# Kernel tuning notes

Hardware: AMD Instinct MI355X
Metric: run time of the kernel (lower is better)

Reference implementation:

```python
import jax, jax.numpy as jnp
import numpy as np

N, D_IN, D_OUT = 4096, 1024, 1024

def setup_inputs() -> dict:
    key = jax.random.key(0)
    k1, k2, k3, k4 = jax.random.split(key, 4)
    x = jax.random.normal(k1, (N, D_IN), dtype=jnp.float32)
    # original uses torch.rand (uniform [0,1)) for params
    w_query = jax.random.uniform(k2, (D_IN, D_OUT), dtype=jnp.float32)
    w_key = jax.random.uniform(k3, (D_IN, D_OUT), dtype=jnp.float32)
    w_value = jax.random.uniform(k4, (D_IN, D_OUT), dtype=jnp.float32)
    return {"x": x, "w_query": w_query, "w_key": w_key, "w_value": w_value}

def reference(x, w_query, w_key, w_value):
    queries = x @ w_query          # [N, d_out]
    keys = x @ w_key               # [N, d_out]
    values = x @ w_value           # [N, d_out]
    scale = keys.shape[-1] ** 0.5
    scores = queries @ keys.T      # [N, N]
    attn = jax.nn.softmax(scores / scale, axis=-1)
    return attn @ values           # [N, d_out]
```

## Files before the change

kernel.cpp:

```cpp
#include <hip/hip_runtime.h>
#include <math.h>

#define NROWS 4096
#define DDIM  1024

typedef __attribute__((ext_vector_type(8))) short short8;
typedef __attribute__((ext_vector_type(4))) float f32x4;

__device__ __forceinline__ ushort f2bf(float v) {
  union { float f; uint32_t u; } c; c.f = v;
  uint32_t u = c.u;
  uint32_t lsb = (u >> 16) & 1u;
  u += 0x7fffu + lsb;
  return (ushort)(u >> 16);
}
__device__ __forceinline__ float bf2f(ushort h) {
  union { uint32_t u; float f; } c; c.u = ((uint32_t)h) << 16;
  return c.f;
}

__device__ __forceinline__ void gll16(const void* g, void* l) {
  __builtin_amdgcn_global_load_lds((const __attribute__((address_space(1))) void*)g,
                                   (__attribute__((address_space(3))) void*)l, 16, 0, 0);
}

__device__ __forceinline__ size_t pidx(int r, int c, int ldt) {
  return ((size_t)((r >> 4) * ldt + (c >> 5))) * 512 +
         ((c >> 3) & 3) * 128 + (r & 15) * 8 + (c & 7);
}
__device__ __forceinline__ size_t pidxs(int r, int c, int ldt) {
  return ((size_t)((r >> 4) * ldt + (c >> 5))) * 1024 +
         ((c >> 3) & 3) * 128 + (r & 15) * 8 + (c & 7);
}

__global__ __launch_bounds__(256) void prep(const float* __restrict__ x,
                                            const float* __restrict__ wq,
                                            const float* __restrict__ wk,
                                            const float* __restrict__ wv,
                                            ushort* Xc,
                                            ushort* Wqc, ushort* Wkc, ushort* Wvh) {
  __shared__ float tl[32][33];
  const int b = blockIdx.x, t = threadIdx.x;
  if (b < 1024) {
    const f32x4* src = (const f32x4*)x;
#pragma unroll
    for (int r = 0; r < 4; ++r) {
      int i = b * 1024 + r * 256 + t;
      int row = i >> 8;
      int c = (i & 255) << 2;
      f32x4 v = __builtin_nontemporal_load(src + i);
      ushort4 h, l;
      h.x = f2bf(v.x); l.x = f2bf(v.x - bf2f(h.x));
      h.y = f2bf(v.y); l.y = f2bf(v.y - bf2f(h.y));
      h.z = f2bf(v.z); l.z = f2bf(v.z - bf2f(h.z));
      h.w = f2bf(v.w); l.w = f2bf(v.w - bf2f(h.w));
      size_t o = pidxs(row, c, DDIM / 32);
      *(ushort4*)(Xc + o) = h;
      *(ushort4*)(Xc + o + 512) = l;
    }
  } else {
    const int z = (b - 1024) >> 10;
    const int tile = (b - 1024) & 1023;
    const float* src = z == 0 ? wq : (z == 1 ? wk : wv);
    const int r0 = (tile >> 5) * 32;
    const int c0 = (tile & 31) * 32;
    const int tx = t & 31, ty = t >> 5;
    for (int i = ty; i < 32; i += 8)
      tl[i][tx] = __builtin_nontemporal_load(&src[(size_t)(r0 + i) * DDIM + c0 + tx]);
    __syncthreads();
    if (z == 2) {
      for (int i = ty; i < 32; i += 8) {
        float v = tl[tx][i];
        Wvh[pidx(c0 + i, r0 + tx, DDIM / 32)] = f2bf(v);
      }
    } else {
      ushort* d = z == 0 ? Wqc : Wkc;
      for (int i = ty; i < 32; i += 8) {
        float v = tl[tx][i];
        ushort h = f2bf(v);
        size_t o = pidxs(c0 + i, r0 + tx, DDIM / 32);
        d[o] = h;
        d[o + 512] = f2bf(v - bf2f(h));
      }
    }
  }
}

template <int MI, bool SPLIT, int KT, int KTOT, int SA, int SB>
__device__ __forceinline__ void direct_gemm(const ushort* __restrict__ A,
                                            const ushort* __restrict__ B,
                                            int m0, int n0, f32x4 (*acc)[4]) {
  const int t = threadIdx.x;
  const int wv = t >> 6, ln = t & 63;
  const int arb = (wv >> 1) * (MI * 16), crb = (wv & 1) * 64;
  const int ra = (m0 + arb) >> 4;
  const int rb = (n0 + crb) >> 4;

  uint oA[MI], oB[4];
#pragma unroll
  for (int i = 0; i < MI; ++i) oA[i] = (uint)(ra + i) * (uint)(KTOT * SA) + (uint)ln * 8u;
#pragma unroll
  for (int j = 0; j < 4; ++j) oB[j] = (uint)(rb + j) * (uint)(KTOT * SB) + (uint)ln * 8u;

  short8 ah0[MI], al0[MI], bh0[4], bl0[4];
  short8 ah1[MI], al1[MI], bh1[4], bl1[4];

#define DG_LOAD(sidx, AH, AL, BH, BL)                                        \
  {                                                                          \
    uint sa_ = (uint)(sidx) * (uint)SA;                                      \
    uint sb_ = (uint)(sidx) * (uint)SB;                                      \
    _Pragma("unroll") for (int i_ = 0; i_ < MI; ++i_) {                      \
      const ushort* pa_ = A + oA[i_] + sa_;                                  \
      AH[i_] = *(const short8*)pa_;                                          \
      if constexpr (SPLIT) AL[i_] = *(const short8*)(pa_ + 512);             \
    }                                                                        \
    _Pragma("unroll") for (int j_ = 0; j_ < 4; ++j_) {                       \
      const ushort* pb_ = B + oB[j_] + sb_;                                  \
      BH[j_] = *(const short8*)pb_;                                          \
      if constexpr (SPLIT) BL[j_] = *(const short8*)(pb_ + 512);             \
    }                                                                        \
  }

#define DG_MFMA(AH, AL, BH, BL)                                              \
  {                                                                          \
    __builtin_amdgcn_s_setprio(1);                                           \
    _Pragma("unroll") for (int j_ = 0; j_ < 4; ++j_) {                       \
      _Pragma("unroll") for (int i_ = 0; i_ < MI; ++i_) {                    \
        acc[i_][j_] = __builtin_amdgcn_mfma_f32_16x16x32_bf16(               \
            AH[i_], BH[j_], acc[i_][j_], 0, 0, 0);                           \
        if constexpr (SPLIT) {                                               \
          acc[i_][j_] = __builtin_amdgcn_mfma_f32_16x16x32_bf16(             \
              AH[i_], BL[j_], acc[i_][j_], 0, 0, 0);                         \
          acc[i_][j_] = __builtin_amdgcn_mfma_f32_16x16x32_bf16(             \
              AL[i_], BH[j_], acc[i_][j_], 0, 0, 0);                         \
        }                                                                    \
      }                                                                      \
    }                                                                        \
    __builtin_amdgcn_s_setprio(0);                                           \
  }

  DG_LOAD(0, ah0, al0, bh0, bl0);
#pragma unroll 1
  for (int s = 0; s < KT - 2; s += 2) {
    DG_LOAD(s + 1, ah1, al1, bh1, bl1);
    DG_MFMA(ah0, al0, bh0, bl0);
    DG_LOAD(s + 2, ah0, al0, bh0, bl0);
    DG_MFMA(ah1, al1, bh1, bl1);
  }
  DG_LOAD(KT - 1, ah1, al1, bh1, bl1);
  DG_MFMA(ah0, al0, bh0, bl0);
  DG_MFMA(ah1, al1, bh1, bl1);

#undef DG_LOAD
#undef DG_MFMA
}

__global__ __launch_bounds__(256) void gemm_qkv(const ushort* __restrict__ Xc,
                                                const ushort* __restrict__ Wqc,
                                                const ushort* __restrict__ Wkc,
                                                const ushort* __restrict__ Wvh,
                                                ushort* Qc, ushort* Kc, ushort* Vt) {
  __shared__ char smem[2][32768];
  const int bid = blockIdx.x;
  const int which = bid >> 8;
  const int local = bid & 255;
  const int xcd = local & 7, idx = local >> 3;
  const int t = threadIdx.x;
  const int w = t >> 6, ln = t & 63;
  const int wr = w >> 1, wc = w & 1;
  const int quad = ln >> 4, l16 = ln & 15;

  f32x4 acc[4][4];
#pragma unroll
  for (int i = 0; i < 4; ++i)
#pragma unroll
    for (int j = 0; j < 4; ++j) acc[i][j] = (f32x4){0.f, 0.f, 0.f, 0.f};

  if (which < 2) {
    const int m0 = (xcd * 4 + (idx >> 3)) * 128;
    const int n0 = (idx & 7) * 128;
    const ushort* Bc = which ? Wkc : Wqc;
    const char* srcBase = (w < 2)
        ? (const char*)Xc + (size_t)((m0 >> 4) + (w & 1) * 4) * 65536
        : (const char*)Bc + (size_t)((n0 >> 4) + (w & 1) * 4) * 65536;
    srcBase += ln * 16;
    char* ldsBase = (char*)smem + (w < 2 ? 0 : 16384) + (w & 1) * 8192 + ln * 16;

#pragma unroll
    for (int u = 0; u < 8; ++u)
      gll16(srcBase + (u >> 1) * 65536 + (u & 1) * 1024, ldsBase + u * 1024);
    asm volatile("s_waitcnt vmcnt(0)" ::: "memory");
    __builtin_amdgcn_s_barrier();

    const char* aB = (char*)smem + wr * 8192 + ln * 16;
    const char* bB = (char*)smem + 16384 + wc * 8192 + ln * 16;

#pragma unroll 1
    for (int kt = 0; kt < 32; ++kt) {
      const int cb = (kt & 1) << 15;
      const int nb = ((kt + 1) & 1) << 15;
      if (kt < 31) {
        const char* srcK = srcBase + (size_t)(kt + 1) * 2048;
#pragma unroll
        for (int u = 0; u < 8; ++u)
          gll16(srcK + (u >> 1) * 65536 + (u & 1) * 1024, ldsBase + nb + u * 1024);
      }

      short8 bh[4], bl[4];
#pragma unroll
      for (int j = 0; j < 4; ++j) {
        bh[j] = *(const short8*)(bB + cb + j * 2048);
        bl[j] = *(const short8*)(bB + cb + j * 2048 + 1024);
      }
      __builtin_amdgcn_s_setprio(1);
#pragma unroll
      for (int i = 0; i < 4; ++i) {
        short8 ah = *(const short8*)(aB + cb + i * 2048);
        short8 al = *(const short8*)(aB + cb + i * 2048 + 1024);
#pragma unroll
        for (int j = 0; j < 4; ++j) {
          acc[i][j] = __builtin_amdgcn_mfma_f32_16x16x32_bf16(ah, bh[j], acc[i][j], 0, 0, 0);
          acc[i][j] = __builtin_amdgcn_mfma_f32_16x16x32_bf16(ah, bl[j], acc[i][j], 0, 0, 0);
          acc[i][j] = __builtin_amdgcn_mfma_f32_16x16x32_bf16(al, bh[j], acc[i][j], 0, 0, 0);
        }
      }
      __builtin_amdgcn_s_setprio(0);

      asm volatile("s_waitcnt vmcnt(0)" ::: "memory");
      __builtin_amdgcn_s_barrier();
    }

    const float scale = which ? 1.0f : 0.03125f;
    ushort* D = which ? Kc : Qc;
#pragma unroll
    for (int i = 0; i < 4; ++i)
#pragma unroll
      for (int j = 0; j < 4; ++j) {
        int col = n0 + wc * 64 + j * 16 + l16;
        int rw = m0 + wr * 64 + i * 16 + quad * 4;
#pragma unroll
        for (int r2 = 0; r2 < 4; ++r2) {
          float v = acc[i][j][r2] * scale;
          ushort h = f2bf(v);
          size_t o = pidxs(rw + r2, col, DDIM / 32);
          D[o] = h;
          D[o + 512] = f2bf(v - bf2f(h));
        }
      }
  } else {
    const int m0 = (idx & 7) * 128;
    const int n0 = (xcd * 4 + (idx >> 3)) * 128;
    const char* srcBase = (w < 2)
        ? (const char*)Wvh + (size_t)((m0 >> 4) + (w & 1) * 4) * 32768
        : (const char*)Xc + (size_t)((n0 >> 4) + (w & 1) * 4) * 65536;
    srcBase += ln * 16;
    char* ldsBase = (char*)smem + (w < 2 ? 0 : 8192) + (w & 1) * 4096 + ln * 16;
    const size_t srcStep = (w < 2) ? 1024 : 2048;
    const size_t rowStr = (w < 2) ? 32768 : 65536;

#pragma unroll
    for (int u = 0; u < 4; ++u)
      gll16(srcBase + (size_t)u * rowStr, ldsBase + u * 1024);
    asm volatile("s_waitcnt vmcnt(0)" ::: "memory");
    __builtin_amdgcn_s_barrier();

    const char* aB = (char*)smem + wr * 4096 + ln * 16;
    const char* bB = (char*)smem + 8192 + wc * 4096 + ln * 16;

#pragma unroll 1
    for (int kt = 0; kt < 32; ++kt) {
      const int cb = (kt & 1) << 15;
      const int nb = ((kt + 1) & 1) << 15;
      if (kt < 31) {
        const char* srcK = srcBase + (size_t)(kt + 1) * srcStep;
#pragma unroll
        for (int u = 0; u < 4; ++u)
          gll16(srcK + (size_t)u * rowStr, ldsBase + nb + u * 1024);
      }

      short8 bh[4];
#pragma unroll
      for (int j = 0; j < 4; ++j)
        bh[j] = *(const short8*)(bB + cb + j * 1024);
      __builtin_amdgcn_s_setprio(1);
#pragma unroll
      for (int i = 0; i < 4; ++i) {
        short8 ah = *(const short8*)(aB + cb + i * 1024);
#pragma unroll
        for (int j = 0; j < 4; ++j)
          acc[i][j] = __builtin_amdgcn_mfma_f32_16x16x32_bf16(ah, bh[j], acc[i][j], 0, 0, 0);
      }
      __builtin_amdgcn_s_setprio(0);

      asm volatile("s_waitcnt vmcnt(0)" ::: "memory");
      __builtin_amdgcn_s_barrier();
    }

#pragma unroll
    for (int i = 0; i < 4; ++i)
#pragma unroll
      for (int j = 0; j < 4; ++j) {
        int kv = n0 + wc * 64 + j * 16 + l16;
        int d = m0 + wr * 64 + i * 16 + quad * 4;
#pragma unroll
        for (int r2 = 0; r2 < 4; ++r2)
          Vt[pidx(d + r2, kv, NROWS / 32)] = f2bf(acc[i][j][r2]);
      }
  }
}

__global__ __launch_bounds__(512) void gemm_s(const ushort* __restrict__ Qc,
                                              const ushort* __restrict__ Kc,
                                              float* __restrict__ S) {
  __shared__ char smem[2][65536];
  const int bid = blockIdx.y * 16 + blockIdx.x;
  const int xcd = bid & 7, local = bid >> 3;
  const int m0 = ((xcd >> 1) * 4 + (local & 3)) * 256;
  const int n0 = ((xcd & 1) * 8 + (local >> 2)) * 256;
  const int t = threadIdx.x;
  const int w = t >> 6, ln = t & 63;
  const int wr = w >> 2, wc = w & 3;
  const int quad = ln >> 4, l16 = ln & 15;

  const char* srcBase = (w < 4)
      ? (const char*)Qc + (size_t)((m0 >> 4) + w * 4) * 65536
      : (const char*)Kc + (size_t)((n0 >> 4) + (w - 4) * 4) * 65536;
  srcBase += ln * 16;
  char* ldsBase = (char*)smem + w * 8192 + ln * 16;

  f32x4 acc[8][4];
#pragma unroll
  for (int i = 0; i < 8; ++i)
#pragma unroll
    for (int j = 0; j < 4; ++j) acc[i][j] = (f32x4){0.f, 0.f, 0.f, 0.f};

#pragma unroll
  for (int u = 0; u < 8; ++u)
    gll16(srcBase + (u >> 1) * 65536 + (u & 1) * 1024, ldsBase + u * 1024);
  asm volatile("s_waitcnt vmcnt(0)" ::: "memory");
  __builtin_amdgcn_s_barrier();

  const char* aB = (char*)smem + (wr * 8) * 2048 + ln * 16;
  const char* bB = (char*)smem + 32768 + (wc * 4) * 2048 + ln * 16;

#pragma unroll 1
  for (int kt = 0; kt < 32; ++kt) {
    const int cb = (kt & 1) << 16;
    const int nb = ((kt + 1) & 1) << 16;
    const char* srcK = srcBase + (size_t)(kt + 1) * 2048;

    if (kt < 31) {
#pragma unroll
      for (int u = 0; u < 8; ++u)
        gll16(srcK + (u >> 1) * 65536 + (u & 1) * 1024, ldsBase + nb + u * 1024);
    }

    short8 bh[4], bl[4];
#pragma unroll
    for (int j = 0; j < 4; ++j) {
      bh[j] = *(const short8*)(bB + cb + j * 2048);
      bl[j] = *(const short8*)(bB + cb + j * 2048 + 1024);
    }

#pragma unroll
    for (int p = 0; p < 4; ++p) {
      short8 ah0 = *(const short8*)(aB + cb + (2 * p) * 2048);
      short8 al0 = *(const short8*)(aB + cb + (2 * p) * 2048 + 1024);
      short8 ah1 = *(const short8*)(aB + cb + (2 * p + 1) * 2048);
      short8 al1 = *(const short8*)(aB + cb + (2 * p + 1) * 2048 + 1024);
      __builtin_amdgcn_s_setprio(1);
#pragma unroll
      for (int j_ = 0; j_ < 4; ++j_) {
        acc[2 * p][j_] = __builtin_amdgcn_mfma_f32_16x16x32_bf16(ah0, bh[j_], acc[2 * p][j_], 0, 0, 0);
        acc[2 * p][j_] = __builtin_amdgcn_mfma_f32_16x16x32_bf16(ah0, bl[j_], acc[2 * p][j_], 0, 0, 0);
        acc[2 * p][j_] = __builtin_amdgcn_mfma_f32_16x16x32_bf16(al0, bh[j_], acc[2 * p][j_], 0, 0, 0);
        acc[2 * p + 1][j_] = __builtin_amdgcn_mfma_f32_16x16x32_bf16(ah1, bh[j_], acc[2 * p + 1][j_], 0, 0, 0);
        acc[2 * p + 1][j_] = __builtin_amdgcn_mfma_f32_16x16x32_bf16(ah1, bl[j_], acc[2 * p + 1][j_], 0, 0, 0);
        acc[2 * p + 1][j_] = __builtin_amdgcn_mfma_f32_16x16x32_bf16(al1, bh[j_], acc[2 * p + 1][j_], 0, 0, 0);
      }
      __builtin_amdgcn_s_setprio(0);
    }

    asm volatile("s_waitcnt vmcnt(0)" ::: "memory");
    __builtin_amdgcn_s_barrier();
  }

#pragma unroll
  for (int i = 0; i < 8; ++i)
#pragma unroll
    for (int j = 0; j < 4; ++j) {
      int col = n0 + wc * 64 + j * 16 + l16;
      int rw = m0 + wr * 128 + i * 16 + quad * 4;
#pragma unroll
      for (int r2 = 0; r2 < 4; ++r2)
        S[(size_t)(rw + r2) * NROWS + col] = acc[i][j][r2];
    }
}

__global__ __launch_bounds__(256) void softmax_pack(const float* __restrict__ S,
                                                    ushort* __restrict__ P) {
  const int row = blockIdx.x, t = threadIdx.x;
  const float* Sr = S + (size_t)row * NROWS;
  const f32x4* S4 = (const f32x4*)Sr;
  f32x4 v[4];
  float mx = -3.4e38f;
#pragma unroll
  for (int c = 0; c < 4; ++c) {
    v[c] = S4[c * 256 + t];
    mx = fmaxf(mx, fmaxf(fmaxf(v[c].x, v[c].y), fmaxf(v[c].z, v[c].w)));
  }
  __shared__ float red[4];
  for (int o = 32; o >= 1; o >>= 1) mx = fmaxf(mx, __shfl_xor(mx, o));
  int wv = t >> 6, ln = t & 63;
  if (ln == 0) red[wv] = mx;
  __syncthreads();
  mx = fmaxf(fmaxf(red[0], red[1]), fmaxf(red[2], red[3]));
  float s = 0.f;
#pragma unroll
  for (int c = 0; c < 4; ++c) {
    v[c].x = __expf(v[c].x - mx);
    v[c].y = __expf(v[c].y - mx);
    v[c].z = __expf(v[c].z - mx);
    v[c].w = __expf(v[c].w - mx);
    s += v[c].x + v[c].y + v[c].z + v[c].w;
  }
  for (int o = 32; o >= 1; o >>= 1) s += __shfl_xor(s, o);
  __syncthreads();
  if (ln == 0) red[wv] = s;
  __syncthreads();
  s = red[0] + red[1] + red[2] + red[3];
  float inv = 1.f / s;
#pragma unroll
  for (int c = 0; c < 4; ++c) {
    ushort4 h;
    h.x = f2bf(v[c].x * inv);
    h.y = f2bf(v[c].y * inv);
    h.z = f2bf(v[c].z * inv);
    h.w = f2bf(v[c].w * inv);
    int c0 = 1024 * c + 4 * t;
    *(ushort4*)(P + pidx(row, c0, NROWS / 32)) = h;
  }
}

__global__ __launch_bounds__(256) void gemm_pv(const ushort* __restrict__ P,
                                               const ushort* __restrict__ Vt,
                                               float* __restrict__ Out) {
  const int n0 = blockIdx.x * 128, m0 = blockIdx.y * 128;
  const int t = threadIdx.x;
  const int wv = t >> 6, ln = t & 63;
  const int quad = ln >> 4, l16 = ln & 15;

  f32x4 acc[4][4];
#pragma unroll
  for (int i = 0; i < 4; ++i)
#pragma unroll
    for (int j = 0; j < 4; ++j) acc[i][j] = (f32x4){0.f, 0.f, 0.f, 0.f};

  direct_gemm<4, false, 128, 128, 512, 512>(P, Vt, m0, n0, acc);

#pragma unroll
  for (int i = 0; i < 4; ++i)
#pragma unroll
    for (int j = 0; j < 4; ++j) {
      int col = n0 + (wv & 1) * 64 + j * 16 + l16;
      int rw = m0 + (wv >> 1) * 64 + i * 16 + quad * 4;
#pragma unroll
      for (int r2 = 0; r2 < 4; ++r2)
        Out[(size_t)(rw + r2) * DDIM + col] = acc[i][j][r2];
    }
}

extern "C" void kernel_launch(void* const* d_in, const int* in_sizes, int n_in,
                              void* d_out, int out_size, void* d_ws, size_t ws_size,
                              hipStream_t stream) {
  const float* x  = (const float*)d_in[0];
  const float* wq = (const float*)d_in[1];
  const float* wk = (const float*)d_in[2];
  const float* wv = (const float*)d_in[3];
  char* ws = (char*)d_ws;
  const size_t MB = 1u << 20;

  ushort* Vt  = (ushort*)(ws + 0);
  ushort* Qc  = (ushort*)(ws + 8 * MB);
  ushort* Kc  = (ushort*)(ws + 24 * MB);
  ushort* Pp  = (ushort*)(ws + 8 * MB);
  ushort* Xc  = (ushort*)(ws + 40 * MB);
  ushort* Wqc = (ushort*)(ws + 56 * MB);
  ushort* Wkc = (ushort*)(ws + 60 * MB);
  ushort* Wvh = (ushort*)(ws + 64 * MB);
  float*  S   = (float*)(ws + 40 * MB);
  float*  Out = (float*)d_out;

  prep<<<4096, 256, 0, stream>>>(x, wq, wk, wv, Xc, Wqc, Wkc, Wvh);
  gemm_qkv<<<768, 256, 0, stream>>>(Xc, Wqc, Wkc, Wvh, Qc, Kc, Vt);
  gemm_s<<<dim3(16, 16), 512, 0, stream>>>(Qc, Kc, S);
  softmax_pack<<<NROWS, 256, 0, stream>>>(S, Pp);
  gemm_pv<<<dim3(8, 32), 256, 0, stream>>>(Pp, Vt, Out);
}
```

Before: 300.5 us.

## Coalesce packed-layout writes via LDS staging and change P layout for PV GEMM

The prep kernel now stages the hi/lo bf16 splits of x and the weights in shared memory, so each block writes whole packed tiles with wide contiguous stores instead of scattered 2-byte and 8-byte writes. Softmax now writes P in a k-tile-major layout with contiguous 16-byte row chunks, and gemm_pv gets its own inlined loader matched to that layout. The gemm_qkv block order is also permuted so the V blocks are scheduled first. These changes target uncoalesced global stores in the pack stages, at the cost of extra LDS traffic and barriers.

```diff
diff --git a/kernel.cpp b/kernel.cpp
--- a/kernel.cpp
+++ b/kernel.cpp
@@ -39,28 +39,45 @@
                                             const float* __restrict__ wv,
                                             ushort* Xc,
                                             ushort* Wqc, ushort* Wkc, ushort* Wvh) {
-  __shared__ float tl[32][33];
+  __shared__ char smem[8448];
   const int b = blockIdx.x, t = threadIdx.x;
-  if (b < 1024) {
-    const f32x4* src = (const f32x4*)x;
-#pragma unroll
-    for (int r = 0; r < 4; ++r) {
-      int i = b * 1024 + r * 256 + t;
-      int row = i >> 8;
-      int c = (i & 255) << 2;
-      f32x4 v = __builtin_nontemporal_load(src + i);
-      ushort4 h, l;
-      h.x = f2bf(v.x); l.x = f2bf(v.x - bf2f(h.x));
-      h.y = f2bf(v.y); l.y = f2bf(v.y - bf2f(h.y));
-      h.z = f2bf(v.z); l.z = f2bf(v.z - bf2f(h.z));
-      h.w = f2bf(v.w); l.w = f2bf(v.w - bf2f(h.w));
-      size_t o = pidxs(row, c, DDIM / 32);
-      *(ushort4*)(Xc + o) = h;
-      *(ushort4*)(Xc + o + 512) = l;
+  if (b < 512) {
+    ushort* xb = (ushort*)smem;
+    const int w = t >> 6, l = t & 63;
+    ushort* wb = xb + w * 1024;
+#pragma unroll 1
+    for (int it = 0; it < 4; ++it) {
+      int tile = b * 16 + it * 4 + w;
+      int tr = tile >> 5, tc = tile & 31;
+      const float* src = x + (size_t)(tr * 16) * DDIM + tc * 32;
+      int r = l >> 3, cq = l & 7;
+#pragma unroll
+      for (int hh = 0; hh < 2; ++hh) {
+        int rr = r + 8 * hh;
+        f32x4 v = __builtin_nontemporal_load(
+            (const f32x4*)(src + (size_t)rr * DDIM) + cq);
+        int c = cq * 4;
+        int intra = ((c >> 3) & 3) * 128 + rr * 8 + (c & 7);
+        ushort4 hi, lo;
+        hi.x = f2bf(v.x); lo.x = f2bf(v.x - bf2f(hi.x));
+        hi.y = f2bf(v.y); lo.y = f2bf(v.y - bf2f(hi.y));
+        hi.z = f2bf(v.z); lo.z = f2bf(v.z - bf2f(hi.z));
+        hi.w = f2bf(v.w); lo.w = f2bf(v.w - bf2f(hi.w));
+        *(ushort4*)(wb + intra) = hi;
+        *(ushort4*)(wb + 512 + intra) = lo;
+      }
+      __syncthreads();
+      ushort* dst = Xc + (size_t)tile * 1024;
+#pragma unroll
+      for (int rd = 0; rd < 2; ++rd)
+        *(short8*)(dst + rd * 512 + l * 8) = *(const short8*)(wb + rd * 512 + l * 8);
+      __syncthreads();
     }
   } else {
-    const int z = (b - 1024) >> 10;
-    const int tile = (b - 1024) & 1023;
+    float (*tl)[33] = (float(*)[33])smem;
+    ushort* stg = (ushort*)(smem + 4224);
+    const int z = (b - 512) >> 10;
+    const int tile = (b - 512) & 1023;
     const float* src = z == 0 ? wq : (z == 1 ? wk : wv);
     const int r0 = (tile >> 5) * 32;
     const int c0 = (tile & 31) * 32;
@@ -68,91 +85,30 @@
     for (int i = ty; i < 32; i += 8)
       tl[i][tx] = __builtin_nontemporal_load(&src[(size_t)(r0 + i) * DDIM + c0 + tx]);
     __syncthreads();
+    const size_t T0 = (size_t)(c0 >> 4) * 32 + (r0 >> 5);
     if (z == 2) {
       for (int i = ty; i < 32; i += 8) {
-        float v = tl[tx][i];
-        Wvh[pidx(c0 + i, r0 + tx, DDIM / 32)] = f2bf(v);
-      }
+        int intra = ((tx >> 3) & 3) * 128 + (i & 15) * 8 + (tx & 7);
+        stg[(i >> 4) * 512 + intra] = f2bf(tl[tx][i]);
+      }
+      __syncthreads();
+      int s = t >> 7, idx = (t & 127) * 4;
+      *(ushort4*)(Wvh + (T0 + (size_t)s * 32) * 512 + idx) = *(const ushort4*)(stg + s * 512 + idx);
     } else {
-      ushort* d = z == 0 ? Wqc : Wkc;
+      ushort* D = z == 0 ? Wqc : Wkc;
       for (int i = ty; i < 32; i += 8) {
         float v = tl[tx][i];
         ushort h = f2bf(v);
-        size_t o = pidxs(c0 + i, r0 + tx, DDIM / 32);
-        d[o] = h;
-        d[o + 512] = f2bf(v - bf2f(h));
-      }
-    }
-  }
-}
-
-template <int MI, bool SPLIT, int KT, int KTOT, int SA, int SB>
-__device__ __forceinline__ void direct_gemm(const ushort* __restrict__ A,
-                                            const ushort* __restrict__ B,
-                                            int m0, int n0, f32x4 (*acc)[4]) {
-  const int t = threadIdx.x;
-  const int wv = t >> 6, ln = t & 63;
-  const int arb = (wv >> 1) * (MI * 16), crb = (wv & 1) * 64;
-  const int ra = (m0 + arb) >> 4;
-  const int rb = (n0 + crb) >> 4;
-
-  uint oA[MI], oB[4];
-#pragma unroll
-  for (int i = 0; i < MI; ++i) oA[i] = (uint)(ra + i) * (uint)(KTOT * SA) + (uint)ln * 8u;
-#pragma unroll
-  for (int j = 0; j < 4; ++j) oB[j] = (uint)(rb + j) * (uint)(KTOT * SB) + (uint)ln * 8u;
-
-  short8 ah0[MI], al0[MI], bh0[4], bl0[4];
-  short8 ah1[MI], al1[MI], bh1[4], bl1[4];
-
-#define DG_LOAD(sidx, AH, AL, BH, BL)                                        \
-  {                                                                          \
-    uint sa_ = (uint)(sidx) * (uint)SA;                                      \
-    uint sb_ = (uint)(sidx) * (uint)SB;                                      \
-    _Pragma("unroll") for (int i_ = 0; i_ < MI; ++i_) {                      \
-      const ushort* pa_ = A + oA[i_] + sa_;                                  \
-      AH[i_] = *(const short8*)pa_;                                          \
-      if constexpr (SPLIT) AL[i_] = *(const short8*)(pa_ + 512);             \
-    }                                                                        \
-    _Pragma("unroll") for (int j_ = 0; j_ < 4; ++j_) {                       \
-      const ushort* pb_ = B + oB[j_] + sb_;                                  \
-      BH[j_] = *(const short8*)pb_;                                          \
-      if constexpr (SPLIT) BL[j_] = *(const short8*)(pb_ + 512);             \
-    }                                                                        \
-  }
-
-#define DG_MFMA(AH, AL, BH, BL)                                              \
-  {                                                                          \
-    __builtin_amdgcn_s_setprio(1);                                           \
-    _Pragma("unroll") for (int j_ = 0; j_ < 4; ++j_) {                       \
-      _Pragma("unroll") for (int i_ = 0; i_ < MI; ++i_) {                    \
-        acc[i_][j_] = __builtin_amdgcn_mfma_f32_16x16x32_bf16(               \
-            AH[i_], BH[j_], acc[i_][j_], 0, 0, 0);                           \
-        if constexpr (SPLIT) {                                               \
-          acc[i_][j_] = __builtin_amdgcn_mfma_f32_16x16x32_bf16(             \
-              AH[i_], BL[j_], acc[i_][j_], 0, 0, 0);                         \
-          acc[i_][j_] = __builtin_amdgcn_mfma_f32_16x16x32_bf16(             \
-              AL[i_], BH[j_], acc[i_][j_], 0, 0, 0);                         \
-        }                                                                    \
-      }                                                                      \
-    }                                                                        \
-    __builtin_amdgcn_s_setprio(0);                                           \
-  }
-
-  DG_LOAD(0, ah0, al0, bh0, bl0);
-#pragma unroll 1
-  for (int s = 0; s < KT - 2; s += 2) {
-    DG_LOAD(s + 1, ah1, al1, bh1, bl1);
-    DG_MFMA(ah0, al0, bh0, bl0);
-    DG_LOAD(s + 2, ah0, al0, bh0, bl0);
-    DG_MFMA(ah1, al1, bh1, bl1);
-  }
-  DG_LOAD(KT - 1, ah1, al1, bh1, bl1);
-  DG_MFMA(ah0, al0, bh0, bl0);
-  DG_MFMA(ah1, al1, bh1, bl1);
-
-#undef DG_LOAD
-#undef DG_MFMA
+        int intra = ((tx >> 3) & 3) * 128 + (i & 15) * 8 + (tx & 7);
+        stg[(i >> 4) * 1024 + intra] = h;
+        stg[(i >> 4) * 1024 + 512 + intra] = f2bf(v - bf2f(h));
+      }
+      __syncthreads();
+      int s = t >> 7, idx = (t & 127) * 8;
+      *(ushort4*)(D + (T0 + (size_t)s * 32) * 1024 + idx) = *(const ushort4*)(stg + s * 1024 + idx);
+      *(ushort4*)(D + (T0 + (size_t)s * 32) * 1024 + idx + 4) = *(const ushort4*)(stg + s * 1024 + idx + 4);
+    }
+  }
 }
 
 __global__ __launch_bounds__(256) void gemm_qkv(const ushort* __restrict__ Xc,
@@ -162,7 +118,7 @@
                                                 ushort* Qc, ushort* Kc, ushort* Vt) {
   __shared__ char smem[2][32768];
   const int bid = blockIdx.x;
-  const int which = bid >> 8;
+  const int which = bid < 256 ? 2 : (bid < 512 ? 0 : 1);
   const int local = bid & 255;
   const int xcd = local & 7, idx = local >> 3;
   const int t = threadIdx.x;
@@ -437,8 +393,8 @@
     h.y = f2bf(v[c].y * inv);
     h.z = f2bf(v[c].z * inv);
     h.w = f2bf(v[c].w * inv);
-    int c0 = 1024 * c + 4 * t;
-    *(ushort4*)(P + pidx(row, c0, NROWS / 32)) = h;
+    int kt = 32 * c + (t >> 3);
+    *(ushort4*)(P + (size_t)kt * 131072 + (size_t)row * 32 + 4 * (t & 7)) = h;
   }
 }
 
@@ -449,6 +405,9 @@
   const int t = threadIdx.x;
   const int wv = t >> 6, ln = t & 63;
   const int quad = ln >> 4, l16 = ln & 15;
+  const int arb = (wv >> 1) * 64, crb = (wv & 1) * 64;
+  const int ra = (m0 + arb) >> 4;
+  const int rb = (n0 + crb) >> 4;
 
   f32x4 acc[4][4];
 #pragma unroll
@@ -456,14 +415,56 @@
 #pragma unroll
     for (int j = 0; j < 4; ++j) acc[i][j] = (f32x4){0.f, 0.f, 0.f, 0.f};
 
-  direct_gemm<4, false, 128, 128, 512, 512>(P, Vt, m0, n0, acc);
-
+  uint oA[4], oB[4];
 #pragma unroll
   for (int i = 0; i < 4; ++i)
+    oA[i] = (uint)(ra + i) * 512u + (uint)(ln & 15) * 32u + (uint)(ln >> 4) * 8u;
+#pragma unroll
+  for (int j = 0; j < 4; ++j)
+    oB[j] = (uint)(rb + j) * 65536u + (uint)ln * 8u;
+
+  short8 a0[4], b0[4], a1[4], b1[4];
+
+#define PV_LOAD(sidx, AH, BH)                                                \
+  {                                                                          \
+    uint ka_ = (uint)(sidx)*131072u;                                         \
+    uint kb_ = (uint)(sidx)*512u;                                            \
+    _Pragma("unroll") for (int i_ = 0; i_ < 4; ++i_)                         \
+      AH[i_] = *(const short8*)(P + oA[i_] + ka_);                           \
+    _Pragma("unroll") for (int j_ = 0; j_ < 4; ++j_)                         \
+      BH[j_] = *(const short8*)(Vt + oB[j_] + kb_);                          \
+  }
+
+#define PV_MFMA(AH, BH)                                                      \
+  {                                                                          \
+    __builtin_amdgcn_s_setprio(1);                                           \
+    _Pragma("unroll") for (int j_ = 0; j_ < 4; ++j_)                         \
+      _Pragma("unroll") for (int i_ = 0; i_ < 4; ++i_)                       \
+        acc[i_][j_] = __builtin_amdgcn_mfma_f32_16x16x32_bf16(               \
+            AH[i_], BH[j_], acc[i_][j_], 0, 0, 0);                           \
+    __builtin_amdgcn_s_setprio(0);                                           \
+  }
+
+  PV_LOAD(0, a0, b0);
+#pragma unroll 1
+  for (int s = 0; s < 126; s += 2) {
+    PV_LOAD(s + 1, a1, b1);
+    PV_MFMA(a0, b0);
+    PV_LOAD(s + 2, a0, b0);
+    PV_MFMA(a1, b1);
+  }
+  PV_LOAD(127, a1, b1);
+  PV_MFMA(a0, b0);
+  PV_MFMA(a1, b1);
+#undef PV_LOAD
+#undef PV_MFMA
+
+#pragma unroll
+  for (int i = 0; i < 4; ++i)
 #pragma unroll
     for (int j = 0; j < 4; ++j) {
-      int col = n0 + (wv & 1) * 64 + j * 16 + l16;
-      int rw = m0 + (wv >> 1) * 64 + i * 16 + quad * 4;
+      int col = n0 + crb + j * 16 + l16;
+      int rw = m0 + arb + i * 16 + quad * 4;
 #pragma unroll
       for (int r2 = 0; r2 < 4; ++r2)
         Out[(size_t)(rw + r2) * DDIM + col] = acc[i][j][r2];
@@ -491,7 +492,7 @@
   float*  S   = (float*)(ws + 40 * MB);
   float*  Out = (float*)d_out;
 
-  prep<<<4096, 256, 0, stream>>>(x, wq, wk, wv, Xc, Wqc, Wkc, Wvh);
+  prep<<<3584, 256, 0, stream>>>(x, wq, wk, wv, Xc, Wqc, Wkc, Wvh);
   gemm_qkv<<<768, 256, 0, stream>>>(Xc, Wqc, Wkc, Wvh, Qc, Kc, Vt);
   gemm_s<<<dim3(16, 16), 512, 0, stream>>>(Qc, Kc, S);
   softmax_pack<<<NROWS, 256, 0, stream>>>(S, Pp);
```

Measured after the change: 284.1 us. -5.5%, faster.
